# Performance work log

Hardware: AMD Instinct MI355X
Metric: run time of the kernel (lower is better)

Reference implementation:

```python
import jax, jax.numpy as jnp
import numpy as np

N = 30000
E = 480000
FEAT = 512
HID = 64
HEADS = 8
NUM_CLASSES = 64
DROPOUT = 0.2
NEG_SLOPE = 0.2


def setup_inputs() -> dict:
    key = jax.random.key(0)
    ks = jax.random.split(key, 10)
    x = jax.random.normal(ks[0], (N, FEAT), dtype=jnp.float32)
    edge_index = jax.random.randint(ks[1], (2, E), 0, N, dtype=jnp.int64)
    s1 = 1.0 / np.sqrt(FEAT)
    s2 = 1.0 / np.sqrt(HEADS * HID)
    W1 = jax.random.normal(ks[2], (FEAT, HEADS * HID), dtype=jnp.float32) * s1
    att_src1 = jax.random.normal(ks[3], (HEADS, HID), dtype=jnp.float32) * s2
    att_dst1 = jax.random.normal(ks[4], (HEADS, HID), dtype=jnp.float32) * s2
    b1 = jnp.zeros((HEADS * HID,), dtype=jnp.float32)
    W2 = jax.random.normal(ks[5], (HEADS * HID, HEADS * NUM_CLASSES), dtype=jnp.float32) * s2
    att_src2 = jax.random.normal(ks[6], (HEADS, NUM_CLASSES), dtype=jnp.float32) * (1.0 / np.sqrt(NUM_CLASSES))
    att_dst2 = jax.random.normal(ks[7], (HEADS, NUM_CLASSES), dtype=jnp.float32) * (1.0 / np.sqrt(NUM_CLASSES))
    b2 = jnp.zeros((NUM_CLASSES,), dtype=jnp.float32)
    return {"x": x, "edge_index": edge_index, "W1": W1, "att_src1": att_src1,
            "att_dst1": att_dst1, "b1": b1, "W2": W2, "att_src2": att_src2,
            "att_dst2": att_dst2, "b2": b2}


def _dropout(x, p, key):
    keep = jax.random.bernoulli(key, 1.0 - p, x.shape)
    return jnp.where(keep, x / (1.0 - p), 0.0).astype(x.dtype)


def _gat_conv(x, src, dst, W, att_src, att_dst, bias, concat):
    # PyG GATConv: linear -> per-edge LeakyReLU attention -> segment softmax over dst -> scatter-sum
    n = x.shape[0]
    H, C = att_src.shape
    xp = (x @ W).reshape(n, H, C)                      # [N,H,C]
    a_s = jnp.einsum('nhc,hc->nh', xp, att_src)        # [N,H]
    a_d = jnp.einsum('nhc,hc->nh', xp, att_dst)        # [N,H]
    e = jax.nn.leaky_relu(a_s[src] + a_d[dst], NEG_SLOPE)  # [E,H]
    # segment softmax over destination neighborhoods
    m = jax.ops.segment_max(e, dst, num_segments=n)    # [N,H]
    m = jnp.where(jnp.isfinite(m), m, 0.0)
    p = jnp.exp(e - m[dst])
    s = jax.ops.segment_sum(p, dst, num_segments=n)    # [N,H]
    alpha = p / (s[dst] + 1e-16)                       # [E,H]
    msg = alpha[:, :, None] * xp[src]                  # [E,H,C]
    out = jax.ops.segment_sum(msg, dst, num_segments=n)  # [N,H,C]
    if concat:
        out = out.reshape(n, H * C)
    else:
        out = out.mean(axis=1)
    return out + bias


def reference(x, edge_index, W1, att_src1, att_dst1, b1, W2, att_src2, att_dst2, b2):
    n = x.shape[0]
    loops = jnp.arange(n, dtype=edge_index.dtype)
    src = jnp.concatenate([edge_index[0], loops])  # add_self_loops=True (PyG default)
    dst = jnp.concatenate([edge_index[1], loops])
    dkey = jax.random.key(42)
    k1, k2 = jax.random.split(dkey)

    h = _dropout(x, DROPOUT, k1)
    h = jax.nn.elu(h)
    h = _gat_conv(h, src, dst, W1, att_src1, att_dst1, b1, concat=True)

    h = _dropout(h, DROPOUT, k2)
    h = jax.nn.elu(h)
    out = _gat_conv(h, src, dst, W2, att_src2, att_dst2, b2, concat=False)
    return out
```

## Files before the change

kernel.cpp:

```cpp
#include <hip/hip_runtime.h>
#include <math.h>

#define HD __host__ __device__

static constexpr int NNODE = 30000;
static constexpr int HH    = 512;
static constexpr int HEADS = 8;
static constexpr int CD    = 64;
static constexpr float SLOPE = 0.2f;
static constexpr int TILE = 128;

typedef unsigned short bf16_t;
typedef __attribute__((ext_vector_type(8))) short short8;
typedef __attribute__((ext_vector_type(4))) float f32x4;
struct alignas(8) US4 { unsigned short x, y, z, w; };

__device__ inline float bf2f(unsigned short h){ return __uint_as_float((unsigned)h << 16); }
__device__ inline unsigned short f2bf_rne(float f){
  unsigned u = __float_as_uint(f);
  unsigned r = (u + 0x7FFFu + ((u >> 16) & 1u)) >> 16;
  return (unsigned short)r;
}

HD inline unsigned rotl32(unsigned v, int s){ return (v<<s) | (v>>(32-s)); }

HD inline void tf2x32(unsigned k0, unsigned k1, unsigned c0, unsigned c1,
                      unsigned &o0, unsigned &o1){
  unsigned ks2 = k0 ^ k1 ^ 0x1BD11BDAu;
  unsigned x0 = c0 + k0, x1 = c1 + k1;
  x0+=x1; x1=rotl32(x1,13); x1^=x0;
  x0+=x1; x1=rotl32(x1,15); x1^=x0;
  x0+=x1; x1=rotl32(x1,26); x1^=x0;
  x0+=x1; x1=rotl32(x1, 6); x1^=x0;
  x0 += k1; x1 += ks2 + 1u;
  x0+=x1; x1=rotl32(x1,17); x1^=x0;
  x0+=x1; x1=rotl32(x1,29); x1^=x0;
  x0+=x1; x1=rotl32(x1,16); x1^=x0;
  x0+=x1; x1=rotl32(x1,24); x1^=x0;
  x0 += ks2; x1 += k0 + 2u;
  x0+=x1; x1=rotl32(x1,13); x1^=x0;
  x0+=x1; x1=rotl32(x1,15); x1^=x0;
  x0+=x1; x1=rotl32(x1,26); x1^=x0;
  x0+=x1; x1=rotl32(x1, 6); x1^=x0;
  x0 += k0; x1 += k1 + 3u;
  x0+=x1; x1=rotl32(x1,17); x1^=x0;
  x0+=x1; x1=rotl32(x1,29); x1^=x0;
  x0+=x1; x1=rotl32(x1,16); x1^=x0;
  x0+=x1; x1=rotl32(x1,24); x1^=x0;
  x0 += k1; x1 += ks2 + 4u;
  x0+=x1; x1=rotl32(x1,13); x1^=x0;
  x0+=x1; x1=rotl32(x1,15); x1^=x0;
  x0+=x1; x1=rotl32(x1,26); x1^=x0;
  x0+=x1; x1=rotl32(x1, 6); x1^=x0;
  x0 += ks2; x1 += k0 + 5u;
  o0 = x0; o1 = x1;
}

__global__ void dropelu_split_kernel(const float* __restrict__ in, const float* __restrict__ bias,
                                     bf16_t* __restrict__ hi, bf16_t* __restrict__ lo,
                                     unsigned key0, unsigned key1, int total4, int width){
  int i = blockIdx.x * blockDim.x + threadIdx.x;
  if (i >= total4) return;
  int e0 = i * 4;
  float4 v4 = *reinterpret_cast<const float4*>(&in[e0]);
  float vv[4] = {v4.x, v4.y, v4.z, v4.w};
  if (bias){
    float4 b4 = *reinterpret_cast<const float4*>(&bias[e0 % width]);
    vv[0]+=b4.x; vv[1]+=b4.y; vv[2]+=b4.z; vv[3]+=b4.w;
  }
  US4 h4, l4;
  unsigned short* hp = &h4.x; unsigned short* lp = &l4.x;
  #pragma unroll
  for (int j = 0; j < 4; ++j){
    unsigned o0, o1;
    tf2x32(key0, key1, 0u, (unsigned)(e0 + j), o0, o1);
    unsigned bits = o0 ^ o1;
    float u = __uint_as_float((bits >> 9) | 0x3f800000u) - 1.0f;
    float v = vv[j];
    v = (u < 0.8f) ? (v * 1.25f) : 0.0f;
    v = (v > 0.0f) ? v : expm1f(v);
    unsigned short hh = f2bf_rne(v);
    hp[j] = hh;
    lp[j] = f2bf_rne(v - bf2f(hh));
  }
  *reinterpret_cast<US4*>(&hi[e0]) = h4;
  *reinterpret_cast<US4*>(&lo[e0]) = l4;
}

__global__ void splitW_kernel(const float* __restrict__ W, bf16_t* __restrict__ Wthi,
                              bf16_t* __restrict__ Wtlo){
  int idx = blockIdx.x * blockDim.x + threadIdx.x;
  if (idx >= 512 * 512) return;
  int j = idx >> 9, k = idx & 511;
  float v = W[k * 512 + j];
  unsigned short hh = f2bf_rne(v);
  Wthi[idx] = hh;
  Wtlo[idx] = f2bf_rne(v - bf2f(hh));
}

#define LSTR 40
__global__ __launch_bounds__(256) void gemm_mfma_kernel(
    const bf16_t* __restrict__ Ahi, const bf16_t* __restrict__ Alo,
    const bf16_t* __restrict__ Bthi, const bf16_t* __restrict__ Btlo,
    float* __restrict__ C, int M){
  __shared__ bf16_t lAhi[128][LSTR], lAlo[128][LSTR], lBhi[128][LSTR], lBlo[128][LSTR];
  int t  = threadIdx.x;
  int bx = blockIdx.x & 3;
  int by = blockIdx.x >> 2;
  int row0 = by * 128, col0 = bx * 128;
  int lane = t & 63, wid = t >> 6;
  int wr = wid >> 1, wc = wid & 1;
  f32x4 acc[4][4] = {};
  int srow  = t >> 1;
  int skoff = (t & 1) * 16;
  int frow = lane & 15, fk = (lane >> 4) * 8;
  for (int k0 = 0; k0 < 512; k0 += 32){
    {
      const bf16_t* pa = &Ahi[(size_t)(row0 + srow) * 512 + k0 + skoff];
      *reinterpret_cast<short8*>(&lAhi[srow][skoff])     = *reinterpret_cast<const short8*>(pa);
      *reinterpret_cast<short8*>(&lAhi[srow][skoff + 8]) = *reinterpret_cast<const short8*>(pa + 8);
      const bf16_t* pl = &Alo[(size_t)(row0 + srow) * 512 + k0 + skoff];
      *reinterpret_cast<short8*>(&lAlo[srow][skoff])     = *reinterpret_cast<const short8*>(pl);
      *reinterpret_cast<short8*>(&lAlo[srow][skoff + 8]) = *reinterpret_cast<const short8*>(pl + 8);
      const bf16_t* pb = &Bthi[(size_t)(col0 + srow) * 512 + k0 + skoff];
      *reinterpret_cast<short8*>(&lBhi[srow][skoff])     = *reinterpret_cast<const short8*>(pb);
      *reinterpret_cast<short8*>(&lBhi[srow][skoff + 8]) = *reinterpret_cast<const short8*>(pb + 8);
      const bf16_t* pc = &Btlo[(size_t)(col0 + srow) * 512 + k0 + skoff];
      *reinterpret_cast<short8*>(&lBlo[srow][skoff])     = *reinterpret_cast<const short8*>(pc);
      *reinterpret_cast<short8*>(&lBlo[srow][skoff + 8]) = *reinterpret_cast<const short8*>(pc + 8);
    }
    __syncthreads();
    short8 fahi[4], falo[4], fbhi[4], fblo[4];
    #pragma unroll
    for (int m = 0; m < 4; ++m){
      fahi[m] = *reinterpret_cast<const short8*>(&lAhi[wr*64 + m*16 + frow][fk]);
      falo[m] = *reinterpret_cast<const short8*>(&lAlo[wr*64 + m*16 + frow][fk]);
    }
    #pragma unroll
    for (int n = 0; n < 4; ++n){
      fbhi[n] = *reinterpret_cast<const short8*>(&lBhi[wc*64 + n*16 + frow][fk]);
      fblo[n] = *reinterpret_cast<const short8*>(&lBlo[wc*64 + n*16 + frow][fk]);
    }
    #pragma unroll
    for (int m = 0; m < 4; ++m)
      #pragma unroll
      for (int n = 0; n < 4; ++n){
        acc[m][n] = __builtin_amdgcn_mfma_f32_16x16x32_bf16(fahi[m], fbhi[n], acc[m][n], 0, 0, 0);
        acc[m][n] = __builtin_amdgcn_mfma_f32_16x16x32_bf16(fahi[m], fblo[n], acc[m][n], 0, 0, 0);
        acc[m][n] = __builtin_amdgcn_mfma_f32_16x16x32_bf16(falo[m], fbhi[n], acc[m][n], 0, 0, 0);
      }
    __syncthreads();
  }
  int rbase = row0 + wr * 64 + (lane >> 4) * 4;
  int cbase = col0 + wc * 64 + (lane & 15);
  #pragma unroll
  for (int m = 0; m < 4; ++m)
    #pragma unroll
    for (int n = 0; n < 4; ++n)
      #pragma unroll
      for (int r = 0; r < 4; ++r){
        int gr = rbase + m * 16 + r;
        if (gr < M) C[(size_t)gr * 512 + cbase + n * 16] = acc[m][n][r];
      }
}

__global__ void attn_coef_kernel(const float* __restrict__ xp, const float* __restrict__ att_src,
                                 const float* __restrict__ att_dst,
                                 float* __restrict__ a_s, float* __restrict__ a_d){
  int wid = (blockIdx.x * blockDim.x + threadIdx.x) >> 6;
  int lane = threadIdx.x & 63;
  if (wid >= NNODE * HEADS) return;
  int n = wid >> 3, h = wid & 7;
  float x  = xp[n * HH + h * CD + lane];
  float vs = x * att_src[h * CD + lane];
  float vd = x * att_dst[h * CD + lane];
  #pragma unroll
  for (int off = 32; off; off >>= 1){
    vs += __shfl_xor(vs, off, 64);
    vd += __shfl_xor(vd, off, 64);
  }
  if (lane == 0){ a_s[wid] = vs; a_d[wid] = vd; }
}

__global__ void init_deg_kernel(int* __restrict__ deg){
  int i = blockIdx.x * blockDim.x + threadIdx.x;
  if (i < NNODE) deg[i] = 1;
}

__global__ void count_deg_kernel(const int* __restrict__ ei, int* __restrict__ deg, int E){
  int t = blockIdx.x * blockDim.x + threadIdx.x;
  if (t < E) atomicAdd(&deg[ei[E + t]], 1);
}

__global__ __launch_bounds__(1024) void scan_kernel(const int* __restrict__ deg,
                                                    int* __restrict__ row_ptr,
                                                    int* __restrict__ cur){
  __shared__ int sums[1024];
  int t = threadIdx.x;
  const int PER = (NNODE + 1023) / 1024;
  int base = t * PER;
  int s = 0;
  for (int i = 0; i < PER; ++i){ int idx = base + i; if (idx < NNODE) s += deg[idx]; }
  sums[t] = s;
  __syncthreads();
  for (int off = 1; off < 1024; off <<= 1){
    int v = (t >= off) ? sums[t - off] : 0;
    __syncthreads();
    sums[t] += v;
    __syncthreads();
  }
  int run = (t == 0) ? 0 : sums[t - 1];
  for (int i = 0; i < PER; ++i){
    int idx = base + i;
    if (idx < NNODE){ row_ptr[idx] = run; cur[idx] = run; run += deg[idx]; }
  }
  if (t == 1023) row_ptr[NNODE] = sums[1023];
}

__global__ void scatter_kernel(const int* __restrict__ ei, int* __restrict__ cur,
                               int* __restrict__ col, int E){
  int t = blockIdx.x * blockDim.x + threadIdx.x;
  int total = E + NNODE;
  if (t >= total) return;
  int src, dst;
  if (t < E){ src = ei[t]; dst = ei[E + t]; }
  else      { src = t - E; dst = t - E; }
  int pos = atomicAdd(&cur[dst], 1);
  col[pos] = src;
}

template <bool CONCAT>
__global__ __launch_bounds__(256) void gat_aggregate2_kernel(
    const int* __restrict__ row_ptr, const int* __restrict__ col,
    const float* __restrict__ a_s, const float* __restrict__ a_d,
    const float* __restrict__ xp, const float* __restrict__ bias,
    float* __restrict__ out){
  int n   = blockIdx.x;
  int tid = threadIdx.x;
  int lane = tid & 63, wslot = tid >> 6;
  int h  = tid & 7;
  int h2 = tid >> 5;
  __shared__ int   scol[TILE];
  __shared__ float sp[TILE][8];
  __shared__ float red[32];
  __shared__ float m_run[8], s_run[8], nm[8], fr[8];
  int start = row_ptr[n], end = row_ptr[n + 1];
  int deg = end - start;
  if (tid < 8){ m_run[tid] = -INFINITY; s_run[tid] = 0.f; }
  float adh = a_d[n * 8 + h];
  float acc0 = 0.f, acc1 = 0.f;
  for (int base = 0; base < deg; base += TILE){
    int len = min(TILE, deg - base);
    __syncthreads();
    if (tid < TILE) scol[tid] = (tid < len) ? col[start + base + tid] : 0;
    __syncthreads();
    float mpart = -INFINITY;
    #pragma unroll
    for (int k = 0; k < TILE * 8 / 256; ++k){
      int j = (tid >> 3) + k * 32;
      float e = -INFINITY;
      if (j < len){
        int src = scol[j];
        e = a_s[src * 8 + h] + adh;
        e = (e >= 0.f) ? e : SLOPE * e;
      }
      sp[j][h] = e;
      mpart = fmaxf(mpart, e);
    }
    #pragma unroll
    for (int off = 8; off < 64; off <<= 1) mpart = fmaxf(mpart, __shfl_xor(mpart, off, 64));
    if (lane < 8) red[wslot * 8 + lane] = mpart;
    __syncthreads();
    if (tid < 8){
      float tm = fmaxf(fmaxf(red[tid], red[8 + tid]), fmaxf(red[16 + tid], red[24 + tid]));
      float om = m_run[tid];
      float nmv = fmaxf(om, tm);
      nm[tid] = nmv;
      fr[tid] = expf(om - nmv);
      m_run[tid] = nmv;
    }
    __syncthreads();
    float nmh = nm[h];
    float spart = 0.f;
    #pragma unroll
    for (int k = 0; k < TILE * 8 / 256; ++k){
      int j = (tid >> 3) + k * 32;
      float p = expf(sp[j][h] - nmh);
      sp[j][h] = p;
      spart += p;
    }
    #pragma unroll
    for (int off = 8; off < 64; off <<= 1) spart += __shfl_xor(spart, off, 64);
    __syncthreads();
    if (lane < 8) red[wslot * 8 + lane] = spart;
    __syncthreads();
    if (tid < 8){
      float ts = red[tid] + red[8 + tid] + red[16 + tid] + red[24 + tid];
      s_run[tid] = s_run[tid] * fr[tid] + ts;
    }
    float facc = fr[h2];
    acc0 *= facc; acc1 *= facc;
    int c0 = 2 * tid;
    for (int j = 0; j < len; ++j){
      float p = sp[j][h2];
      int src = scol[j];
      float2 v = *reinterpret_cast<const float2*>(&xp[(size_t)src * 512 + c0]);
      acc0 += p * v.x; acc1 += p * v.y;
    }
  }
  __syncthreads();
  if (CONCAT){
    float inv = 1.0f / (s_run[h2] + 1e-16f);
    float2 o = make_float2(acc0 * inv, acc1 * inv);
    *reinterpret_cast<float2*>(&out[(size_t)n * 512 + 2 * tid]) = o;
  } else {
    float inv = 0.125f / (s_run[h2] + 1e-16f);
    float* fbuf = &sp[0][0];
    fbuf[2 * tid]     = acc0 * inv;
    fbuf[2 * tid + 1] = acc1 * inv;
    __syncthreads();
    if (tid < 64){
      float s = 0.f;
      #pragma unroll
      for (int hh = 0; hh < 8; ++hh) s += fbuf[hh * 64 + tid];
      out[(size_t)n * 64 + tid] = s + bias[tid];
    }
  }
}

extern "C" void kernel_launch(void* const* d_in, const int* in_sizes, int n_in,
                              void* d_out, int out_size, void* d_ws, size_t ws_size,
                              hipStream_t stream){
  const float* x   = (const float*)d_in[0];
  const int*   ei  = (const int*)  d_in[1];
  const float* W1  = (const float*)d_in[2];
  const float* as1 = (const float*)d_in[3];
  const float* ad1 = (const float*)d_in[4];
  const float* b1  = (const float*)d_in[5];
  const float* W2  = (const float*)d_in[6];
  const float* as2 = (const float*)d_in[7];
  const float* ad2 = (const float*)d_in[8];
  const float* b2  = (const float*)d_in[9];
  float* out = (float*)d_out;
  const int E = in_sizes[1] / 2;
  const int EN = E + NNODE;

  char* w = (char*)d_ws;
  bf16_t* Ahi = (bf16_t*)w; w += (size_t)NNODE * HH * 2;
  bf16_t* Alo = (bf16_t*)w; w += (size_t)NNODE * HH * 2;
  float* xp   = (float*)w;  w += (size_t)NNODE * HH * 4;
  float* o1   = (float*)w;  w += (size_t)NNODE * HH * 4;
  bf16_t* Wt1hi = (bf16_t*)w; w += (size_t)512 * 512 * 2;
  bf16_t* Wt1lo = (bf16_t*)w; w += (size_t)512 * 512 * 2;
  bf16_t* Wt2hi = (bf16_t*)w; w += (size_t)512 * 512 * 2;
  bf16_t* Wt2lo = (bf16_t*)w; w += (size_t)512 * 512 * 2;
  float* a_s  = (float*)w; w += (size_t)NNODE * HEADS * 4;
  float* a_d  = (float*)w; w += (size_t)NNODE * HEADS * 4;
  int* deg     = (int*)w; w += (size_t)NNODE * 4;
  int* row_ptr = (int*)w; w += (size_t)(NNODE + 1) * 4;
  int* cur     = (int*)w; w += (size_t)NNODE * 4;
  int* col     = (int*)w; w += (size_t)EN * 4;

  unsigned k1a, k1b, k2a, k2b;
  tf2x32(0u, 42u, 0u, 0u, k1a, k1b);
  tf2x32(0u, 42u, 0u, 1u, k2a, k2b);

  const int total4 = NNODE * HH / 4;
  const int gemm_grid = ((NNODE + 127) / 128) * 4;

  splitW_kernel<<<1024, 256, 0, stream>>>(W1, Wt1hi, Wt1lo);
  splitW_kernel<<<1024, 256, 0, stream>>>(W2, Wt2hi, Wt2lo);
  init_deg_kernel<<<(NNODE + 255) / 256, 256, 0, stream>>>(deg);
  count_deg_kernel<<<(E + 255) / 256, 256, 0, stream>>>(ei, deg, E);
  scan_kernel<<<1, 1024, 0, stream>>>(deg, row_ptr, cur);
  scatter_kernel<<<(EN + 255) / 256, 256, 0, stream>>>(ei, cur, col, E);

  dropelu_split_kernel<<<(total4 + 255) / 256, 256, 0, stream>>>(x, nullptr, Ahi, Alo, k1a, k1b, total4, HH);
  gemm_mfma_kernel<<<gemm_grid, 256, 0, stream>>>(Ahi, Alo, Wt1hi, Wt1lo, xp, NNODE);
  attn_coef_kernel<<<(NNODE * HEADS + 3) / 4, 256, 0, stream>>>(xp, as1, ad1, a_s, a_d);
  gat_aggregate2_kernel<true><<<NNODE, 256, 0, stream>>>(row_ptr, col, a_s, a_d, xp, nullptr, o1);

  dropelu_split_kernel<<<(total4 + 255) / 256, 256, 0, stream>>>(o1, b1, Ahi, Alo, k2a, k2b, total4, HH);
  gemm_mfma_kernel<<<gemm_grid, 256, 0, stream>>>(Ahi, Alo, Wt2hi, Wt2lo, xp, NNODE);
  attn_coef_kernel<<<(NNODE * HEADS + 3) / 4, 256, 0, stream>>>(xp, as2, ad2, a_s, a_d);
  gat_aggregate2_kernel<false><<<NNODE, 256, 0, stream>>>(row_ptr, col, a_s, a_d, xp, b2, out);
}
```

Measured before the change: 767.7 us.

## Fuse attention coefficients into GEMM epilogue and store projected features as bf16

Computes a_s/a_d directly from the GEMM accumulators in the epilogue, which removes the separate attn_coef kernel and its read of xp. Projected features are now stored as bf16, halving the bytes the gather-heavy aggregation reads per neighbour. The aggregation splits the edge loop across two thread groups, each handling 4 channels, and combines them through shared memory. The two weight-split launches are merged into one. The cost is lower precision in the aggregated features, and the partial-sum reduction adds an extra shared-memory pass.

```diff
diff --git a/kernel.cpp b/kernel.cpp
--- a/kernel.cpp
+++ b/kernel.cpp
@@ -87,22 +87,28 @@
   *reinterpret_cast<US4*>(&lo[e0]) = l4;
 }
 
-__global__ void splitW_kernel(const float* __restrict__ W, bf16_t* __restrict__ Wthi,
-                              bf16_t* __restrict__ Wtlo){
+__global__ void splitW2_kernel(const float* __restrict__ W1, const float* __restrict__ W2,
+                               bf16_t* __restrict__ Wt1hi, bf16_t* __restrict__ Wt1lo,
+                               bf16_t* __restrict__ Wt2hi, bf16_t* __restrict__ Wt2lo){
   int idx = blockIdx.x * blockDim.x + threadIdx.x;
-  if (idx >= 512 * 512) return;
-  int j = idx >> 9, k = idx & 511;
+  int which = idx >> 18;
+  int r = idx & ((1 << 18) - 1);
+  int j = r >> 9, k = r & 511;
+  const float* W = which ? W2 : W1;
+  bf16_t* Whi = which ? Wt2hi : Wt1hi;
+  bf16_t* Wlo = which ? Wt2lo : Wt1lo;
   float v = W[k * 512 + j];
   unsigned short hh = f2bf_rne(v);
-  Wthi[idx] = hh;
-  Wtlo[idx] = f2bf_rne(v - bf2f(hh));
+  Whi[r] = hh;
+  Wlo[r] = f2bf_rne(v - bf2f(hh));
 }
 
 #define LSTR 40
-__global__ __launch_bounds__(256) void gemm_mfma_kernel(
+__global__ __launch_bounds__(256) void gemm_mfma_fused_kernel(
     const bf16_t* __restrict__ Ahi, const bf16_t* __restrict__ Alo,
     const bf16_t* __restrict__ Bthi, const bf16_t* __restrict__ Btlo,
-    float* __restrict__ C, int M){
+    const float* __restrict__ att_src, const float* __restrict__ att_dst,
+    bf16_t* __restrict__ xpb, float* __restrict__ a_s, float* __restrict__ a_d, int M){
   __shared__ bf16_t lAhi[128][LSTR], lAlo[128][LSTR], lBhi[128][LSTR], lBlo[128][LSTR];
   int t  = threadIdx.x;
   int bx = blockIdx.x & 3;
@@ -160,26 +166,36 @@
       #pragma unroll
       for (int r = 0; r < 4; ++r){
         int gr = rbase + m * 16 + r;
-        if (gr < M) C[(size_t)gr * 512 + cbase + n * 16] = acc[m][n][r];
-      }
-}
-
-__global__ void attn_coef_kernel(const float* __restrict__ xp, const float* __restrict__ att_src,
-                                 const float* __restrict__ att_dst,
-                                 float* __restrict__ a_s, float* __restrict__ a_d){
-  int wid = (blockIdx.x * blockDim.x + threadIdx.x) >> 6;
-  int lane = threadIdx.x & 63;
-  if (wid >= NNODE * HEADS) return;
-  int n = wid >> 3, h = wid & 7;
-  float x  = xp[n * HH + h * CD + lane];
-  float vs = x * att_src[h * CD + lane];
-  float vd = x * att_dst[h * CD + lane];
+        if (gr < M) xpb[(size_t)gr * 512 + cbase + n * 16] = f2bf_rne(acc[m][n][r]);
+      }
+  int hh = 2 * bx + wc;
+  float as_c[4], ad_c[4];
   #pragma unroll
-  for (int off = 32; off; off >>= 1){
-    vs += __shfl_xor(vs, off, 64);
-    vd += __shfl_xor(vd, off, 64);
-  }
-  if (lane == 0){ a_s[wid] = vs; a_d[wid] = vd; }
+  for (int n = 0; n < 4; ++n){
+    as_c[n] = att_src[hh * 64 + n * 16 + (lane & 15)];
+    ad_c[n] = att_dst[hh * 64 + n * 16 + (lane & 15)];
+  }
+  #pragma unroll
+  for (int m = 0; m < 4; ++m)
+    #pragma unroll
+    for (int r = 0; r < 4; ++r){
+      float ps = 0.f, pd = 0.f;
+      #pragma unroll
+      for (int n = 0; n < 4; ++n){
+        ps += acc[m][n][r] * as_c[n];
+        pd += acc[m][n][r] * ad_c[n];
+      }
+      #pragma unroll
+      for (int off = 1; off < 16; off <<= 1){
+        ps += __shfl_xor(ps, off, 64);
+        pd += __shfl_xor(pd, off, 64);
+      }
+      int row = row0 + wr * 64 + m * 16 + (lane >> 4) * 4 + r;
+      if ((lane & 15) == 0 && row < M){
+        a_s[row * 8 + hh] = ps;
+        a_d[row * 8 + hh] = pd;
+      }
+    }
 }
 
 __global__ void init_deg_kernel(int* __restrict__ deg){
@@ -230,25 +246,29 @@
 }
 
 template <bool CONCAT>
-__global__ __launch_bounds__(256) void gat_aggregate2_kernel(
+__global__ __launch_bounds__(256) void gat_aggregate3_kernel(
     const int* __restrict__ row_ptr, const int* __restrict__ col,
     const float* __restrict__ a_s, const float* __restrict__ a_d,
-    const float* __restrict__ xp, const float* __restrict__ bias,
+    const bf16_t* __restrict__ xpb, const float* __restrict__ bias,
     float* __restrict__ out){
   int n   = blockIdx.x;
   int tid = threadIdx.x;
   int lane = tid & 63, wslot = tid >> 6;
   int h  = tid & 7;
-  int h2 = tid >> 5;
+  int g  = tid >> 7;
+  int local = tid & 127;
+  int c0 = local * 4;
+  int h2 = local >> 4;
   __shared__ int   scol[TILE];
   __shared__ float sp[TILE][8];
   __shared__ float red[32];
   __shared__ float m_run[8], s_run[8], nm[8], fr[8];
+  __shared__ float xacc[512];
   int start = row_ptr[n], end = row_ptr[n + 1];
   int deg = end - start;
   if (tid < 8){ m_run[tid] = -INFINITY; s_run[tid] = 0.f; }
   float adh = a_d[n * 8 + h];
-  float acc0 = 0.f, acc1 = 0.f;
+  float a0 = 0.f, a1 = 0.f, a2 = 0.f, a3 = 0.f;
   for (int base = 0; base < deg; base += TILE){
     int len = min(TILE, deg - base);
     __syncthreads();
@@ -298,31 +318,38 @@
       float ts = red[tid] + red[8 + tid] + red[16 + tid] + red[24 + tid];
       s_run[tid] = s_run[tid] * fr[tid] + ts;
     }
-    float facc = fr[h2];
-    acc0 *= facc; acc1 *= facc;
-    int c0 = 2 * tid;
-    for (int j = 0; j < len; ++j){
+    float f = fr[h2];
+    a0 *= f; a1 *= f; a2 *= f; a3 *= f;
+    for (int j = g; j < len; j += 2){
       float p = sp[j][h2];
       int src = scol[j];
-      float2 v = *reinterpret_cast<const float2*>(&xp[(size_t)src * 512 + c0]);
-      acc0 += p * v.x; acc1 += p * v.y;
+      US4 v = *reinterpret_cast<const US4*>(&xpb[(size_t)src * 512 + c0]);
+      a0 += p * bf2f(v.x); a1 += p * bf2f(v.y);
+      a2 += p * bf2f(v.z); a3 += p * bf2f(v.w);
     }
   }
   __syncthreads();
-  if (CONCAT){
-    float inv = 1.0f / (s_run[h2] + 1e-16f);
-    float2 o = make_float2(acc0 * inv, acc1 * inv);
-    *reinterpret_cast<float2*>(&out[(size_t)n * 512 + 2 * tid]) = o;
-  } else {
-    float inv = 0.125f / (s_run[h2] + 1e-16f);
-    float* fbuf = &sp[0][0];
-    fbuf[2 * tid]     = acc0 * inv;
-    fbuf[2 * tid + 1] = acc1 * inv;
+  if (g == 1){
+    xacc[c0] = a0; xacc[c0+1] = a1; xacc[c0+2] = a2; xacc[c0+3] = a3;
+  }
+  __syncthreads();
+  if (g == 0){
+    a0 += xacc[c0]; a1 += xacc[c0+1]; a2 += xacc[c0+2]; a3 += xacc[c0+3];
+    if (CONCAT){
+      float inv = 1.0f / (s_run[h2] + 1e-16f);
+      float4 o = make_float4(a0*inv, a1*inv, a2*inv, a3*inv);
+      *reinterpret_cast<float4*>(&out[(size_t)n * 512 + c0]) = o;
+    } else {
+      float inv = 0.125f / (s_run[h2] + 1e-16f);
+      xacc[c0] = a0*inv; xacc[c0+1] = a1*inv; xacc[c0+2] = a2*inv; xacc[c0+3] = a3*inv;
+    }
+  }
+  if (!CONCAT){
     __syncthreads();
     if (tid < 64){
       float s = 0.f;
       #pragma unroll
-      for (int hh = 0; hh < 8; ++hh) s += fbuf[hh * 64 + tid];
+      for (int hh = 0; hh < 8; ++hh) s += xacc[hh * 64 + tid];
       out[(size_t)n * 64 + tid] = s + bias[tid];
     }
   }
@@ -348,7 +375,7 @@
   char* w = (char*)d_ws;
   bf16_t* Ahi = (bf16_t*)w; w += (size_t)NNODE * HH * 2;
   bf16_t* Alo = (bf16_t*)w; w += (size_t)NNODE * HH * 2;
-  float* xp   = (float*)w;  w += (size_t)NNODE * HH * 4;
+  bf16_t* xpb = (bf16_t*)w; w += (size_t)NNODE * HH * 2;
   float* o1   = (float*)w;  w += (size_t)NNODE * HH * 4;
   bf16_t* Wt1hi = (bf16_t*)w; w += (size_t)512 * 512 * 2;
   bf16_t* Wt1lo = (bf16_t*)w; w += (size_t)512 * 512 * 2;
@@ -368,20 +395,17 @@
   const int total4 = NNODE * HH / 4;
   const int gemm_grid = ((NNODE + 127) / 128) * 4;
 
-  splitW_kernel<<<1024, 256, 0, stream>>>(W1, Wt1hi, Wt1lo);
-  splitW_kernel<<<1024, 256, 0, stream>>>(W2, Wt2hi, Wt2lo);
+  splitW2_kernel<<<2048, 256, 0, stream>>>(W1, W2, Wt1hi, Wt1lo, Wt2hi, Wt2lo);
   init_deg_kernel<<<(NNODE + 255) / 256, 256, 0, stream>>>(deg);
   count_deg_kernel<<<(E + 255) / 256, 256, 0, stream>>>(ei, deg, E);
   scan_kernel<<<1, 1024, 0, stream>>>(deg, row_ptr, cur);
   scatter_kernel<<<(EN + 255) / 256, 256, 0, stream>>>(ei, cur, col, E);
 
   dropelu_split_kernel<<<(total4 + 255) / 256, 256, 0, stream>>>(x, nullptr, Ahi, Alo, k1a, k1b, total4, HH);
-  gemm_mfma_kernel<<<gemm_grid, 256, 0, stream>>>(Ahi, Alo, Wt1hi, Wt1lo, xp, NNODE);
-  attn_coef_kernel<<<(NNODE * HEADS + 3) / 4, 256, 0, stream>>>(xp, as1, ad1, a_s, a_d);
-  gat_aggregate2_kernel<true><<<NNODE, 256, 0, stream>>>(row_ptr, col, a_s, a_d, xp, nullptr, o1);
+  gemm_mfma_fused_kernel<<<gemm_grid, 256, 0, stream>>>(Ahi, Alo, Wt1hi, Wt1lo, as1, ad1, xpb, a_s, a_d, NNODE);
+  gat_aggregate3_kernel<true><<<NNODE, 256, 0, stream>>>(row_ptr, col, a_s, a_d, xpb, nullptr, o1);
 
   dropelu_split_kernel<<<(total4 + 255) / 256, 256, 0, stream>>>(o1, b1, Ahi, Alo, k2a, k2b, total4, HH);
-  gemm_mfma_kernel<<<gemm_grid, 256, 0, stream>>>(Ahi, Alo, Wt2hi, Wt2lo, xp, NNODE);
-  attn_coef_kernel<<<(NNODE * HEADS + 3) / 4, 256, 0, stream>>>(xp, as2, ad2, a_s, a_d);
-  gat_aggregate2_kernel<false><<<NNODE, 256, 0, stream>>>(row_ptr, col, a_s, a_d, xp, b2, out);
-}
+  gemm_mfma_fused_kernel<<<gemm_grid, 256, 0, stream>>>(Ahi, Alo, Wt2hi, Wt2lo, as2, ad2, xpb, a_s, a_d, NNODE);
+  gat_aggregate3_kernel<false><<<NNODE, 256, 0, stream>>>(row_ptr, col, a_s, a_d, xpb, b2, out);
+}
```

New measurement: 616.0 us. -19.8%, faster.
